# Kernel tuning notes

Hardware: AMD Instinct MI355X
Metric: run time of the kernel (lower is better)

## Reference

```python
import jax, jax.numpy as jnp
import numpy as np

N = 100_000      # nodes
E = 1_600_000    # edges (before self-loops)
IN = 128         # in_dim
H = 4            # heads (layer 1)
C = 32           # hidden_dim (per-head channels)
ED = 16          # edge_dim
NEG_SLOPE = 0.2  # PyG GATConv default


def setup_inputs() -> dict:
    key = jax.random.key(0)
    ks = jax.random.split(key, 16)
    s = 0.05
    return {
        "x": jax.random.normal(ks[0], (N, IN), jnp.float32),
        "edge_index": jax.random.randint(ks[1], (2, E), 0, N, dtype=jnp.int32),
        "edge_attr": jax.random.normal(ks[2], (E, ED), jnp.float32),
        # layer 1 params (heads=H, concat=True)
        "W1": jax.random.normal(ks[3], (IN, H * C), jnp.float32) * s,
        "W1e": jax.random.normal(ks[4], (ED, H * C), jnp.float32) * s,
        "a1_src": jax.random.normal(ks[5], (H, C), jnp.float32) * s,
        "a1_dst": jax.random.normal(ks[6], (H, C), jnp.float32) * s,
        "a1_edge": jax.random.normal(ks[7], (H, C), jnp.float32) * s,
        "b1": jax.random.normal(ks[8], (H * C,), jnp.float32) * s,
        # layer 2 params (heads=1, concat=False)
        "W2": jax.random.normal(ks[9], (H * C, C), jnp.float32) * s,
        "W2e": jax.random.normal(ks[10], (ED, C), jnp.float32) * s,
        "a2_src": jax.random.normal(ks[11], (1, C), jnp.float32) * s,
        "a2_dst": jax.random.normal(ks[12], (1, C), jnp.float32) * s,
        "a2_edge": jax.random.normal(ks[13], (1, C), jnp.float32) * s,
        "b2": jax.random.normal(ks[14], (C,), jnp.float32) * s,
    }


def _add_self_loops(src, dst, edge_attr, n):
    # PyG GATConv: add_self_loops=True, fill_value='mean' -> self-loop edge_attr
    # is the mean of incoming edge attrs per target node.
    deg = jax.ops.segment_sum(jnp.ones_like(dst, jnp.float32), dst, num_segments=n)
    mean_attr = jax.ops.segment_sum(edge_attr, dst, num_segments=n) / jnp.maximum(deg, 1.0)[:, None]
    loop = jnp.arange(n, dtype=src.dtype)
    src2 = jnp.concatenate([src, loop])
    dst2 = jnp.concatenate([dst, loop])
    attr2 = jnp.concatenate([edge_attr, mean_attr], axis=0)
    return src2, dst2, attr2


def _gat_conv(x, src, dst, eattr, W, We, a_s, a_d, a_e, b, concat):
    n = x.shape[0]
    Hh, Cc = a_s.shape
    h = (x @ W).reshape(n, Hh, Cc)                # [N,H,C]
    he = (eattr @ We).reshape(-1, Hh, Cc)          # [E',H,C]
    al_s = jnp.sum(h * a_s, axis=-1)               # [N,H]
    al_d = jnp.sum(h * a_d, axis=-1)               # [N,H]
    al_e = jnp.sum(he * a_e, axis=-1)              # [E',H]
    e = jax.nn.leaky_relu(al_s[src] + al_d[dst] + al_e, NEG_SLOPE)  # [E',H]
    # segment softmax over destination node neighborhoods
    m = jax.ops.segment_max(e, dst, num_segments=n)                 # [N,H]
    p = jnp.exp(e - m[dst])
    z = jax.ops.segment_sum(p, dst, num_segments=n)                 # [N,H]
    alpha = p / z[dst]                                              # [E',H]
    out = jax.ops.segment_sum(alpha[:, :, None] * h[src], dst, num_segments=n)  # [N,H,C]
    if concat:
        out = out.reshape(n, Hh * Cc)
    else:
        out = out.mean(axis=1)
    return out + b, alpha


def reference(x, edge_index, edge_attr,
              W1, W1e, a1_src, a1_dst, a1_edge, b1,
              W2, W2e, a2_src, a2_dst, a2_edge, b2):
    n = x.shape[0]
    src, dst, eattr = _add_self_loops(edge_index[0], edge_index[1], edge_attr, n)
    h1, _ = _gat_conv(x, src, dst, eattr, W1, W1e, a1_src, a1_dst, a1_edge, b1, concat=True)
    h1 = jax.nn.elu(h1)
    # dropout p applied in training only; inference reference -> identity
    h2, alpha2 = _gat_conv(h1, src, dst, eattr, W2, W2e, a2_src, a2_dst, a2_edge, b2, concat=False)
    h2 = jax.nn.elu(h2)
    edge_index_sl = jnp.stack([src, dst])
    return h2, edge_index_sl, alpha2
```

## Files before the change

kernel.cpp:

```cpp
#include <hip/hip_runtime.h>

#define NN 100000
#define NE 1600000
#define NE2 1700000
#define OUT_EI 3200000
#define OUT_AL 6600000
#define SLOPE 0.2f
#define NB 391
#define EPB 6400
#define NBB 250

typedef unsigned short u16;
typedef unsigned int u32;
typedef __bf16 bf16x8 __attribute__((ext_vector_type(8)));
typedef float f32x4 __attribute__((ext_vector_type(4)));
typedef u32 u32x4 __attribute__((ext_vector_type(4)));

__device__ __forceinline__ float bf2f(u16 u){ return __uint_as_float(((u32)u) << 16); }
__device__ __forceinline__ u16 f2bf(float f){
    u32 x = __float_as_uint(f);
    x += 0x7FFFu + ((x >> 16) & 1u);
    return (u16)(x >> 16);
}
__device__ __forceinline__ float eluf(float v){ return v > 0.f ? v : (__expf(v) - 1.f); }
__device__ __forceinline__ float lreluf(float v){ return fmaxf(v, SLOPE * v); }
__device__ __forceinline__ float sel4f(float a, float b, float c, float d, int s){
    float x = (s & 1) ? b : a;
    float y = (s & 1) ? d : c;
    return (s & 2) ? y : x;
}

__global__ __launch_bounds__(256) void k_bhist(const int* __restrict__ ei, int* __restrict__ bcnt){
    __shared__ int s[NB];
    int t = threadIdx.x;
    for (int i = t; i < NB; i += 256) s[i] = 0;
    __syncthreads();
    int e0 = blockIdx.x * EPB;
    for (int i = t; i < EPB; i += 256)
        atomicAdd(&s[ei[NE + e0 + i] >> 8], 1);
    __syncthreads();
    for (int i = t; i < NB; i += 256) if (s[i]) atomicAdd(&bcnt[i], s[i]);
}

__global__ void k_bscan(const int* __restrict__ bcnt, int* __restrict__ bbase, int* __restrict__ bcur){
    __shared__ int s[512];
    int t = threadIdx.x;
    int v = (t < NB) ? bcnt[t] : 0;
    s[t] = v; __syncthreads();
    #pragma unroll
    for (int d = 1; d < 512; d <<= 1){
        int x = (t >= d) ? s[t - d] : 0;
        __syncthreads();
        s[t] += x;
        __syncthreads();
    }
    if (t < NB){ int ex = s[t] - v; bbase[t] = ex; bcur[t] = ex; }
    if (t == 0) bbase[NB] = NE;
}

__global__ __launch_bounds__(256) void k_bscatter(const int* __restrict__ ei, const u16* __restrict__ ale1,
                                                  const u16* __restrict__ ale2,
                                                  int* __restrict__ bcur, u32* __restrict__ binsP,
                                                  uint2* __restrict__ binsA, u16* __restrict__ binsA2){
    __shared__ int cnt[NB];
    __shared__ int base[NB];
    __shared__ int sdst[EPB];
    int t = threadIdx.x;
    for (int i = t; i < NB; i += 256) cnt[i] = 0;
    __syncthreads();
    int e0 = blockIdx.x * EPB;
    for (int i = t; i < EPB; i += 256){
        int dv = ei[NE + e0 + i];
        sdst[i] = dv;
        atomicAdd(&cnt[dv >> 8], 1);
    }
    __syncthreads();
    for (int i = t; i < NB; i += 256){
        int c = cnt[i];
        base[i] = c ? atomicAdd(&bcur[i], c) : 0;
        cnt[i] = 0;
    }
    __syncthreads();
    const uint2* a1 = (const uint2*)ale1;
    for (int i = t; i < EPB; i += 256){
        int e = e0 + i;
        int dst = sdst[i];
        int b = dst >> 8;
        int r = atomicAdd(&cnt[b], 1);
        int pos = base[b] + r;
        binsP[pos] = ((u32)(dst & 255) << 24) | (u32)ei[e];
        binsA[pos] = a1[e];
        binsA2[pos] = ale2[e];
    }
}

__global__ __launch_bounds__(256) void k_fscatter(const u32* __restrict__ binsP, const uint2* __restrict__ binsA,
                                                  const u16* __restrict__ binsA2, const int* __restrict__ bbase,
                                                  int* __restrict__ offsets,
                                                  int* __restrict__ src32, uint2* __restrict__ ale1p,
                                                  u16* __restrict__ ale2p){
    __shared__ int d[256];
    __shared__ int s[256];
    __shared__ int cur[256];
    int t = threadIdx.x, b = blockIdx.x;
    d[t] = 0;
    __syncthreads();
    int bs = bbase[b], be = bbase[b + 1];
    for (int i = bs + t; i < be; i += 256)
        atomicAdd(&d[binsP[i] >> 24], 1);
    __syncthreads();
    int v = d[t];
    s[t] = v; __syncthreads();
    #pragma unroll
    for (int dd = 1; dd < 256; dd <<= 1){
        int x = (t >= dd) ? s[t - dd] : 0;
        __syncthreads();
        s[t] += x;
        __syncthreads();
    }
    int n = b * 256 + t;
    int off = bs + (s[t] - v) + n;
    if (n < NN) offsets[n] = off;
    cur[t] = off + 1;
    if (b == 0 && t == 0) offsets[NN] = NE + NN;
    __syncthreads();
    for (int i = bs + t; i < be; i += 256){
        u32 p = binsP[i];
        int dl = p >> 24;
        int pos = atomicAdd(&cur[dl], 1);
        src32[pos] = (int)(p & 0xFFFFFFu);
        ale1p[pos] = binsA[i];
        ale2p[pos] = binsA2[i];
    }
}

__global__ void k_q(const float* __restrict__ W1e, const float* __restrict__ a1e,
                    const float* __restrict__ W2e, const float* __restrict__ a2e,
                    float* __restrict__ q1, float* __restrict__ q2){
    int t = threadIdx.x;
    int k = t >> 2, h = t & 3;
    float s = 0.f;
    for (int c = 0; c < 32; c++) s += W1e[k * 128 + h * 32 + c] * a1e[h * 32 + c];
    q1[t] = s;
    if (t < 16){
        float s2 = 0.f;
        for (int c = 0; c < 32; c++) s2 += W2e[t * 32 + c] * a2e[c];
        q2[t] = s2;
    }
}

__global__ __launch_bounds__(256) void k_ale(const float* __restrict__ eattr,
                                             const float* __restrict__ q1, const float* __restrict__ q2,
                                             u16* __restrict__ ale1, u16* __restrict__ ale2){
    __shared__ float sq1[64], sq2[16];
    int t = threadIdx.x;
    if (t < 64) sq1[t] = q1[t];
    if (t < 16) sq2[t] = q2[t];
    __syncthreads();
    int gt = blockIdx.x * 256 + t;
    int e = gt >> 2, part = gt & 3;
    f32x4 av = ((const f32x4*)eattr)[(size_t)e * 4 + part];
    int j0 = part * 4;
    float p0 = 0, p1 = 0, p2 = 0, p3 = 0, p4 = 0;
    #pragma unroll
    for (int k = 0; k < 4; k++){
        float a = av[k]; int j = j0 + k;
        p0 += a * sq1[j * 4 + 0]; p1 += a * sq1[j * 4 + 1];
        p2 += a * sq1[j * 4 + 2]; p3 += a * sq1[j * 4 + 3];
        p4 += a * sq2[j];
    }
    #pragma unroll
    for (int m = 1; m < 4; m <<= 1){
        p0 += __shfl_xor(p0, m); p1 += __shfl_xor(p1, m);
        p2 += __shfl_xor(p2, m); p3 += __shfl_xor(p3, m); p4 += __shfl_xor(p4, m);
    }
    if (part == 0){
        ushort4 w; w.x = f2bf(p0); w.y = f2bf(p1); w.z = f2bf(p2); w.w = f2bf(p3);
        ((ushort4*)ale1)[e] = w;
        ale2[e] = f2bf(p4);
    }
}

__global__ __launch_bounds__(256) void k_gemm1(const float* __restrict__ x, const float* __restrict__ W,
                                               const float* __restrict__ a1s, const float* __restrict__ a1d,
                                               u16* __restrict__ h1,
                                               float* __restrict__ al_s, float* __restrict__ al_d){
    __shared__ __align__(16) u16 sW[128 * 136];
    int t = threadIdx.x;
    for (int i = t; i < 128 * 128; i += 256){
        int k = i >> 7, c = i & 127;
        sW[c * 136 + k] = f2bf(W[i]);
    }
    __syncthreads();
    int lane = t & 63, wave = t >> 6;
    int quad = lane >> 4, m16 = lane & 15;
    int rowA = blockIdx.x * 64 + wave * 16 + m16;
    bf16x8 afr[4];
    if (rowA < NN){
        const f32x4* xr = (const f32x4*)(x + (size_t)rowA * 128);
        #pragma unroll
        for (int kk = 0; kk < 4; kk++){
            f32x4 va = xr[kk * 8 + quad * 2];
            f32x4 vb = xr[kk * 8 + quad * 2 + 1];
            #pragma unroll
            for (int i2 = 0; i2 < 4; i2++){ afr[kk][i2] = (__bf16)va[i2]; afr[kk][4 + i2] = (__bf16)vb[i2]; }
        }
    } else {
        #pragma unroll
        for (int kk = 0; kk < 4; kk++)
            #pragma unroll
            for (int i2 = 0; i2 < 8; i2++) afr[kk][i2] = (__bf16)0.f;
    }
    int rowbase = blockIdx.x * 64 + wave * 16 + quad * 4;
    float vsA[4][4], vdA[4][4];
    #pragma unroll
    for (int r = 0; r < 4; r++)
        #pragma unroll
        for (int h = 0; h < 4; h++){ vsA[r][h] = 0.f; vdA[r][h] = 0.f; }
    #pragma unroll
    for (int nt = 0; nt < 8; nt++){
        f32x4 acc = (f32x4){0.f, 0.f, 0.f, 0.f};
        const u16* wp = &sW[(nt * 16 + m16) * 136 + quad * 8];
        #pragma unroll
        for (int kk = 0; kk < 4; kk++){
            bf16x8 bfr = *(const bf16x8*)(wp + kk * 32);
            acc = __builtin_amdgcn_mfma_f32_16x16x32_bf16(afr[kk], bfr, acc, 0, 0, 0);
        }
        int col = nt * 16 + m16;
        float cs = a1s[col], cd = a1d[col];
        const int h = nt >> 1;
        #pragma unroll
        for (int r = 0; r < 4; r++){
            vsA[r][h] += acc[r] * cs;
            vdA[r][h] += acc[r] * cd;
            int row = rowbase + r;
            if (row < NN) h1[(size_t)row * 128 + col] = f2bf(acc[r]);
        }
    }
    #pragma unroll
    for (int r = 0; r < 4; r++)
        #pragma unroll
        for (int h = 0; h < 4; h++)
            #pragma unroll
            for (int m = 1; m < 16; m <<= 1){
                vsA[r][h] += __shfl_xor(vsA[r][h], m);
                vdA[r][h] += __shfl_xor(vdA[r][h], m);
            }
    int rs = m16 >> 2, hs = m16 & 3;
    float s0 = sel4f(vsA[0][0], vsA[0][1], vsA[0][2], vsA[0][3], hs);
    float s1 = sel4f(vsA[1][0], vsA[1][1], vsA[1][2], vsA[1][3], hs);
    float s2 = sel4f(vsA[2][0], vsA[2][1], vsA[2][2], vsA[2][3], hs);
    float s3 = sel4f(vsA[3][0], vsA[3][1], vsA[3][2], vsA[3][3], hs);
    float d0 = sel4f(vdA[0][0], vdA[0][1], vdA[0][2], vdA[0][3], hs);
    float d1 = sel4f(vdA[1][0], vdA[1][1], vdA[1][2], vdA[1][3], hs);
    float d2 = sel4f(vdA[2][0], vdA[2][1], vdA[2][2], vdA[2][3], hs);
    float d3 = sel4f(vdA[3][0], vdA[3][1], vdA[3][2], vdA[3][3], hs);
    float souts = sel4f(s0, s1, s2, s3, rs);
    float soutd = sel4f(d0, d1, d2, d3, rs);
    int row = rowbase + rs;
    if (row < NN){
        al_s[row * 4 + hs] = souts;
        al_d[row * 4 + hs] = soutd;
    }
}

__global__ __launch_bounds__(256) void k_gemm2(const u16* __restrict__ hin, const float* __restrict__ W,
                                               const float* __restrict__ a2s, const float* __restrict__ a2d,
                                               float* __restrict__ h2a,
                                               float* __restrict__ al_s, float* __restrict__ al_d){
    __shared__ __align__(16) u16 sW[32 * 136];
    int t = threadIdx.x;
    for (int i = t; i < 128 * 32; i += 256){
        int k = i >> 5, c = i & 31;
        sW[c * 136 + k] = f2bf(W[i]);
    }
    __syncthreads();
    int lane = t & 63, wave = t >> 6;
    int quad = lane >> 4, m16 = lane & 15;
    int rowA = blockIdx.x * 64 + wave * 16 + m16;
    bf16x8 afr[4];
    if (rowA < NN){
        const u16* xr = hin + (size_t)rowA * 128 + quad * 8;
        #pragma unroll
        for (int kk = 0; kk < 4; kk++) afr[kk] = *(const bf16x8*)(xr + kk * 32);
    } else {
        #pragma unroll
        for (int kk = 0; kk < 4; kk++)
            #pragma unroll
            for (int i2 = 0; i2 < 8; i2++) afr[kk][i2] = (__bf16)0.f;
    }
    int rowbase = blockIdx.x * 64 + wave * 16 + quad * 4;
    float vs2[4], vd2[4];
    #pragma unroll
    for (int r = 0; r < 4; r++){ vs2[r] = 0.f; vd2[r] = 0.f; }
    #pragma unroll
    for (int nt = 0; nt < 2; nt++){
        f32x4 acc = (f32x4){0.f, 0.f, 0.f, 0.f};
        const u16* wp = &sW[(nt * 16 + m16) * 136 + quad * 8];
        #pragma unroll
        for (int kk = 0; kk < 4; kk++){
            bf16x8 bfr = *(const bf16x8*)(wp + kk * 32);
            acc = __builtin_amdgcn_mfma_f32_16x16x32_bf16(afr[kk], bfr, acc, 0, 0, 0);
        }
        int col = nt * 16 + m16;
        float cs = a2s[col], cd = a2d[col];
        #pragma unroll
        for (int r = 0; r < 4; r++){
            vs2[r] += acc[r] * cs;
            vd2[r] += acc[r] * cd;
            int row = rowbase + r;
            if (row < NN) h2a[(size_t)row * 32 + col] = acc[r];
        }
    }
    #pragma unroll
    for (int r = 0; r < 4; r++)
        #pragma unroll
        for (int m = 1; m < 16; m <<= 1){
            vs2[r] += __shfl_xor(vs2[r], m);
            vd2[r] += __shfl_xor(vd2[r], m);
        }
    if (m16 < 4){
        int row = rowbase + m16;
        if (row < NN){
            al_s[row] = sel4f(vs2[0], vs2[1], vs2[2], vs2[3], m16);
            al_d[row] = sel4f(vd2[0], vd2[1], vd2[2], vd2[3], m16);
        }
    }
}

__global__ __launch_bounds__(256) void k_node1(const int* __restrict__ src32, const u16* __restrict__ ale1u,
                                               const int* __restrict__ offsets,
                                               const float* __restrict__ al_s, const float* __restrict__ al_d,
                                               const u16* __restrict__ h1, const float* __restrict__ b1,
                                               u16* __restrict__ h1b){
    int wave = threadIdx.x >> 6, lane = threadIdx.x & 63;
    int n = blockIdx.x * 4 + wave;
    int start = offsets[n], end = offsets[n + 1];
    int degr = end - start - 1;
    int g = lane >> 4, l = lane & 15, hq = l >> 2;
    float aldh = al_d[n * 4 + hq];
    const u32x4* h1v = (const u32x4*)h1;
    float acc[8];
    #pragma unroll
    for (int k = 0; k < 8; k++) acc[k] = 0.f;
    float z = 0.f, sa = 0.f;
    int i = start + 1 + g;
    int src = (i < end) ? __builtin_nontemporal_load(src32 + i) : 0;
    for (; i < end; i += 4){
        int ni = i + 4;
        int nsrc = (ni < end) ? __builtin_nontemporal_load(src32 + ni) : 0;
        float a = bf2f(__builtin_nontemporal_load(ale1u + (size_t)i * 4 + hq));
        float als = al_s[src * 4 + hq];
        u32x4 v = h1v[(size_t)src * 16 + l];
        float e = __expf(lreluf(als + aldh + a));
        z += e; sa += a;
        #pragma unroll
        for (int k = 0; k < 4; k++){
            acc[2 * k]     += e * bf2f((u16)(v[k] & 0xFFFFu));
            acc[2 * k + 1] += e * bf2f((u16)(v[k] >> 16));
        }
        src = nsrc;
    }
    z += __shfl_xor(z, 16); z += __shfl_xor(z, 32);
    sa += __shfl_xor(sa, 16); sa += __shfl_xor(sa, 32);
    float inv_deg = 1.f / fmaxf((float)degr, 1.f);
    float ps = __expf(lreluf(al_s[n * 4 + hq] + aldh + sa * inv_deg));
    z += ps;
    if (g == 0){
        u32x4 v = h1v[(size_t)n * 16 + l];
        #pragma unroll
        for (int k = 0; k < 4; k++){
            acc[2 * k]     += ps * bf2f((u16)(v[k] & 0xFFFFu));
            acc[2 * k + 1] += ps * bf2f((u16)(v[k] >> 16));
        }
    }
    #pragma unroll
    for (int k = 0; k < 8; k++){
        acc[k] += __shfl_xor(acc[k], 16);
        acc[k] += __shfl_xor(acc[k], 32);
    }
    if (g == 0){
        float rz = 1.f / z;
        u32x4 w;
        #pragma unroll
        for (int k = 0; k < 4; k++){
            float v0 = eluf(acc[2 * k]     * rz + b1[l * 8 + 2 * k]);
            float v1 = eluf(acc[2 * k + 1] * rz + b1[l * 8 + 2 * k + 1]);
            w[k] = (u32)f2bf(v0) | ((u32)f2bf(v1) << 16);
        }
        ((u32x4*)h1b)[(size_t)n * 16 + l] = w;
    }
}

__global__ __launch_bounds__(256) void k_node2(const int* __restrict__ src32, const u16* __restrict__ ale2p,
                                               const int* __restrict__ offsets,
                                               const float* __restrict__ al_s, const float* __restrict__ al_d,
                                               const float* __restrict__ h2a, const float* __restrict__ b2,
                                               float* __restrict__ dout, float* __restrict__ rzv){
    int wave = threadIdx.x >> 6, lane = threadIdx.x & 63;
    int n = blockIdx.x * 4 + wave;
    int start = offsets[n], end = offsets[n + 1];
    int degr = end - start - 1;
    float aldn = al_d[n];
    int g = lane >> 3, l = lane & 7;
    const f32x4* h2v = (const f32x4*)h2a;
    f32x4 acc = (f32x4){0.f, 0.f, 0.f, 0.f};
    float z = 0.f, sa = 0.f;
    int i = start + 1 + g;
    int src = (i < end) ? __builtin_nontemporal_load(src32 + i) : 0;
    for (; i < end; i += 8){
        int ni = i + 8;
        int nsrc = (ni < end) ? __builtin_nontemporal_load(src32 + ni) : 0;
        float a = bf2f(__builtin_nontemporal_load(ale2p + i));
        float als = al_s[src];
        f32x4 v = h2v[(size_t)src * 8 + l];
        float e = __expf(lreluf(als + aldn + a));
        z += e; sa += a;
        #pragma unroll
        for (int k = 0; k < 4; k++) acc[k] += e * v[k];
        src = nsrc;
    }
    z += __shfl_xor(z, 8); z += __shfl_xor(z, 16); z += __shfl_xor(z, 32);
    sa += __shfl_xor(sa, 8); sa += __shfl_xor(sa, 16); sa += __shfl_xor(sa, 32);
    float mal = sa / fmaxf((float)degr, 1.f);
    float ps = __expf(lreluf(al_s[n] + aldn + mal));
    z += ps;
    float rz = 1.f / z;
    if (g == 0){
        f32x4 v = h2v[(size_t)n * 8 + l];
        #pragma unroll
        for (int k = 0; k < 4; k++) acc[k] += ps * v[k];
    }
    if (lane == 0){
        rzv[n] = rz;
        dout[OUT_AL + NE + n] = ps * rz;
        dout[OUT_EI + NE + n] = (float)n;
        dout[OUT_EI + NE2 + NE + n] = (float)n;
    }
    #pragma unroll
    for (int k = 0; k < 4; k++){
        acc[k] += __shfl_xor(acc[k], 8);
        acc[k] += __shfl_xor(acc[k], 16);
        acc[k] += __shfl_xor(acc[k], 32);
    }
    if (g == 0){
        f32x4 w;
        #pragma unroll
        for (int k = 0; k < 4; k++) w[k] = eluf(acc[k] + b2[l * 4 + k]);
        ((f32x4*)dout)[(size_t)n * 8 + l] = w;
    }
}

__global__ __launch_bounds__(256) void k_alpha(const int* __restrict__ ei, const u16* __restrict__ ale2,
                                               const float* __restrict__ al_s, const float* __restrict__ al_d,
                                               const float* __restrict__ rzv, float* __restrict__ dout){
    int e = blockIdx.x * 256 + threadIdx.x;
    int src = ei[e], dst = ei[NE + e];
    float a = bf2f(ale2[e]);
    float ev = __expf(lreluf(al_s[src] + al_d[dst] + a));
    __builtin_nontemporal_store(ev * rzv[dst], &dout[OUT_AL + e]);
    __builtin_nontemporal_store((float)src, &dout[OUT_EI + e]);
    __builtin_nontemporal_store((float)dst, &dout[OUT_EI + NE2 + e]);
}

extern "C" void kernel_launch(void* const* d_in, const int* in_sizes, int n_in,
                              void* d_out, int out_size, void* d_ws, size_t ws_size,
                              hipStream_t stream) {
    const float* x     = (const float*)d_in[0];
    const int*   ei    = (const int*)d_in[1];
    const float* eattr = (const float*)d_in[2];
    const float* W1    = (const float*)d_in[3];
    const float* W1e   = (const float*)d_in[4];
    const float* a1s   = (const float*)d_in[5];
    const float* a1d   = (const float*)d_in[6];
    const float* a1e   = (const float*)d_in[7];
    const float* b1    = (const float*)d_in[8];
    const float* W2    = (const float*)d_in[9];
    const float* W2e   = (const float*)d_in[10];
    const float* a2s   = (const float*)d_in[11];
    const float* a2d   = (const float*)d_in[12];
    const float* a2e   = (const float*)d_in[13];
    const float* b2    = (const float*)d_in[14];
    float* dout = (float*)d_out;

    char* ws = (char*)d_ws;
    size_t off = 0;
    auto alloc = [&](size_t bytes) -> void* {
        void* p = ws + off;
        off += (bytes + 255) & ~(size_t)255;
        return p;
    };
    int* bcnt = (int*)alloc((size_t)NB * 4);
    size_t zero_bytes = off;
    int*     offsets = (int*)alloc((size_t)(NN + 1) * 4);
    int*     bbase   = (int*)alloc((size_t)(NB + 1) * 4);
    int*     bcur    = (int*)alloc((size_t)NB * 4);
    u32*     binsP   = (u32*)alloc((size_t)NE * 4);
    uint2*   binsA   = (uint2*)alloc((size_t)NE * 8);
    u16*     binsA2  = (u16*)alloc((size_t)NE * 2);
    int*     src32   = (int*)alloc((size_t)NE2 * 4);
    uint2*   ale1p   = (uint2*)alloc((size_t)NE2 * 8);
    u16*     ale2p   = (u16*)alloc((size_t)NE2 * 2);
    float*   q1      = (float*)alloc(64 * 4);
    float*   q2      = (float*)alloc(16 * 4);
    u16*     ale1    = (u16*)alloc((size_t)NE * 4 * 2);
    u16*     ale2    = (u16*)alloc((size_t)NE * 2);
    float*   al_s1   = (float*)alloc((size_t)NN * 4 * 4);
    float*   al_d1   = (float*)alloc((size_t)NN * 4 * 4);
    u16*     h1      = (u16*)alloc((size_t)NN * 128 * 2);
    u16*     h1b     = (u16*)alloc((size_t)NN * 128 * 2);
    char*  h1r   = (char*)h1;
    float* h2a   = (float*)(h1r);
    float* al_s2 = (float*)(h1r + 12800000);
    float* al_d2 = (float*)(h1r + 13200128);
    float* rzv   = (float*)(h1r + 13600256);

    const int TB = 256;
    hipMemsetAsync(d_ws, 0, zero_bytes, stream);

    k_q<<<1, 64, 0, stream>>>(W1e, a1e, W2e, a2e, q1, q2);
    k_ale<<<NE * 4 / TB, TB, 0, stream>>>(eattr, q1, q2, ale1, ale2);
    k_bhist<<<NBB, TB, 0, stream>>>(ei, bcnt);
    k_bscan<<<1, 512, 0, stream>>>(bcnt, bbase, bcur);
    k_bscatter<<<NBB, TB, 0, stream>>>(ei, ale1, ale2, bcur, binsP, binsA, binsA2);
    k_fscatter<<<NB, TB, 0, stream>>>(binsP, binsA, binsA2, bbase, offsets, src32, ale1p, ale2p);
    k_gemm1<<<(NN + 63) / 64, TB, 0, stream>>>(x, W1, a1s, a1d, h1, al_s1, al_d1);
    k_node1<<<NN / 4, TB, 0, stream>>>(src32, (const u16*)ale1p, offsets, al_s1, al_d1, h1, b1, h1b);
    k_gemm2<<<(NN + 63) / 64, TB, 0, stream>>>(h1b, W2, a2s, a2d, h2a, al_s2, al_d2);
    k_node2<<<NN / 4, TB, 0, stream>>>(src32, ale2p, offsets, al_s2, al_d2, h2a, b2, dout, rzv);
    k_alpha<<<NE / TB, TB, 0, stream>>>(ei, ale2, al_s2, al_d2, rzv, dout);
}
```

Measured before the change: 562.1 us.

## Fuse layer-2 projection into layer-1 aggregation and software-pipeline gather loops

Removes the separate k_gemm2 launch by computing h1 @ W2 and the layer-2 attention logits inside k_node1, using shared-memory copies of W2 and the per-node h1 row. This avoids writing the bf16 h1b buffer and reading it back. The gather loops in both node kernels are restructured to prefetch one edge ahead (source index, logit and feature row), and layer 1 now uses 8 edge groups with 16 channels per lane. The trade-offs are that every block reloads W2 (16 KB) into shared memory, the projection runs as scalar FP32 FMAs instead of MFMA, and a __syncthreads is added. Layer-2 buffers are also re-aliased onto the bin scratch arrays.

Measured after the change: 591.2 us. +5.2%, slower.

```diff
diff --git a/kernel.cpp b/kernel.cpp
--- a/kernel.cpp
+++ b/kernel.cpp
@@ -9,6 +9,7 @@
 #define NB 391
 #define EPB 6400
 #define NBB 250
+#define NNP 100096
 
 typedef unsigned short u16;
 typedef unsigned int u32;
@@ -264,131 +265,106 @@
     }
 }
 
-__global__ __launch_bounds__(256) void k_gemm2(const u16* __restrict__ hin, const float* __restrict__ W,
-                                               const float* __restrict__ a2s, const float* __restrict__ a2d,
-                                               float* __restrict__ h2a,
-                                               float* __restrict__ al_s, float* __restrict__ al_d){
-    __shared__ __align__(16) u16 sW[32 * 136];
-    int t = threadIdx.x;
-    for (int i = t; i < 128 * 32; i += 256){
-        int k = i >> 5, c = i & 31;
-        sW[c * 136 + k] = f2bf(W[i]);
-    }
-    __syncthreads();
-    int lane = t & 63, wave = t >> 6;
-    int quad = lane >> 4, m16 = lane & 15;
-    int rowA = blockIdx.x * 64 + wave * 16 + m16;
-    bf16x8 afr[4];
-    if (rowA < NN){
-        const u16* xr = hin + (size_t)rowA * 128 + quad * 8;
-        #pragma unroll
-        for (int kk = 0; kk < 4; kk++) afr[kk] = *(const bf16x8*)(xr + kk * 32);
-    } else {
-        #pragma unroll
-        for (int kk = 0; kk < 4; kk++)
-            #pragma unroll
-            for (int i2 = 0; i2 < 8; i2++) afr[kk][i2] = (__bf16)0.f;
-    }
-    int rowbase = blockIdx.x * 64 + wave * 16 + quad * 4;
-    float vs2[4], vd2[4];
-    #pragma unroll
-    for (int r = 0; r < 4; r++){ vs2[r] = 0.f; vd2[r] = 0.f; }
-    #pragma unroll
-    for (int nt = 0; nt < 2; nt++){
-        f32x4 acc = (f32x4){0.f, 0.f, 0.f, 0.f};
-        const u16* wp = &sW[(nt * 16 + m16) * 136 + quad * 8];
-        #pragma unroll
-        for (int kk = 0; kk < 4; kk++){
-            bf16x8 bfr = *(const bf16x8*)(wp + kk * 32);
-            acc = __builtin_amdgcn_mfma_f32_16x16x32_bf16(afr[kk], bfr, acc, 0, 0, 0);
-        }
-        int col = nt * 16 + m16;
-        float cs = a2s[col], cd = a2d[col];
-        #pragma unroll
-        for (int r = 0; r < 4; r++){
-            vs2[r] += acc[r] * cs;
-            vd2[r] += acc[r] * cd;
-            int row = rowbase + r;
-            if (row < NN) h2a[(size_t)row * 32 + col] = acc[r];
-        }
-    }
-    #pragma unroll
-    for (int r = 0; r < 4; r++)
-        #pragma unroll
-        for (int m = 1; m < 16; m <<= 1){
-            vs2[r] += __shfl_xor(vs2[r], m);
-            vd2[r] += __shfl_xor(vd2[r], m);
-        }
-    if (m16 < 4){
-        int row = rowbase + m16;
-        if (row < NN){
-            al_s[row] = sel4f(vs2[0], vs2[1], vs2[2], vs2[3], m16);
-            al_d[row] = sel4f(vd2[0], vd2[1], vd2[2], vd2[3], m16);
-        }
-    }
-}
-
 __global__ __launch_bounds__(256) void k_node1(const int* __restrict__ src32, const u16* __restrict__ ale1u,
                                                const int* __restrict__ offsets,
                                                const float* __restrict__ al_s, const float* __restrict__ al_d,
                                                const u16* __restrict__ h1, const float* __restrict__ b1,
-                                               u16* __restrict__ h1b){
-    int wave = threadIdx.x >> 6, lane = threadIdx.x & 63;
+                                               const float* __restrict__ W2,
+                                               const float* __restrict__ a2s, const float* __restrict__ a2d,
+                                               float* __restrict__ h2a,
+                                               float* __restrict__ al_s2, float* __restrict__ al_d2){
+    __shared__ float sW2[128 * 32];
+    __shared__ float sh1[4][128];
+    int t = threadIdx.x;
+    for (int i = t; i < 128 * 32; i += 256) sW2[i] = W2[i];
+    int wave = t >> 6, lane = t & 63;
     int n = blockIdx.x * 4 + wave;
     int start = offsets[n], end = offsets[n + 1];
     int degr = end - start - 1;
-    int g = lane >> 4, l = lane & 15, hq = l >> 2;
+    int g = lane >> 3, l = lane & 7, hq = l >> 1;
     float aldh = al_d[n * 4 + hq];
     const u32x4* h1v = (const u32x4*)h1;
-    float acc[8];
-    #pragma unroll
-    for (int k = 0; k < 8; k++) acc[k] = 0.f;
+    float acc[16];
+    #pragma unroll
+    for (int k = 0; k < 16; k++) acc[k] = 0.f;
     float z = 0.f, sa = 0.f;
     int i = start + 1 + g;
-    int src = (i < end) ? __builtin_nontemporal_load(src32 + i) : 0;
-    for (; i < end; i += 4){
-        int ni = i + 4;
-        int nsrc = (ni < end) ? __builtin_nontemporal_load(src32 + ni) : 0;
-        float a = bf2f(__builtin_nontemporal_load(ale1u + (size_t)i * 4 + hq));
-        float als = al_s[src * 4 + hq];
-        u32x4 v = h1v[(size_t)src * 16 + l];
-        float e = __expf(lreluf(als + aldh + a));
-        z += e; sa += a;
+    int i1 = i + 8, i2 = i + 16;
+    int src0 = (i  < end) ? __builtin_nontemporal_load(src32 + i)  : n;
+    int src1 = (i1 < end) ? __builtin_nontemporal_load(src32 + i1) : n;
+    float a0   = (i < end) ? bf2f(__builtin_nontemporal_load(ale1u + (size_t)i * 4 + hq)) : 0.f;
+    float als0 = al_s[src0 * 4 + hq];
+    u32x4 v00 = h1v[(size_t)src0 * 16 + 2 * l];
+    u32x4 v01 = h1v[(size_t)src0 * 16 + 2 * l + 1];
+    while (i < end){
+        int src2 = (i2 < end) ? __builtin_nontemporal_load(src32 + i2) : n;
+        float a1v   = (i1 < end) ? bf2f(__builtin_nontemporal_load(ale1u + (size_t)i1 * 4 + hq)) : 0.f;
+        float als1 = al_s[src1 * 4 + hq];
+        u32x4 v10 = h1v[(size_t)src1 * 16 + 2 * l];
+        u32x4 v11 = h1v[(size_t)src1 * 16 + 2 * l + 1];
+        float e = __expf(lreluf(als0 + aldh + a0));
+        z += e; sa += a0;
         #pragma unroll
         for (int k = 0; k < 4; k++){
-            acc[2 * k]     += e * bf2f((u16)(v[k] & 0xFFFFu));
-            acc[2 * k + 1] += e * bf2f((u16)(v[k] >> 16));
+            acc[2 * k]     += e * bf2f((u16)(v00[k] & 0xFFFFu));
+            acc[2 * k + 1] += e * bf2f((u16)(v00[k] >> 16));
+            acc[8 + 2 * k] += e * bf2f((u16)(v01[k] & 0xFFFFu));
+            acc[9 + 2 * k] += e * bf2f((u16)(v01[k] >> 16));
         }
-        src = nsrc;
-    }
-    z += __shfl_xor(z, 16); z += __shfl_xor(z, 32);
-    sa += __shfl_xor(sa, 16); sa += __shfl_xor(sa, 32);
+        i = i1; i1 = i2; i2 += 8;
+        src1 = src2; a0 = a1v; als0 = als1; v00 = v10; v01 = v11;
+    }
+    z += __shfl_xor(z, 8); z += __shfl_xor(z, 16); z += __shfl_xor(z, 32);
+    sa += __shfl_xor(sa, 8); sa += __shfl_xor(sa, 16); sa += __shfl_xor(sa, 32);
     float inv_deg = 1.f / fmaxf((float)degr, 1.f);
     float ps = __expf(lreluf(al_s[n * 4 + hq] + aldh + sa * inv_deg));
     z += ps;
     if (g == 0){
-        u32x4 v = h1v[(size_t)n * 16 + l];
+        u32x4 s0 = h1v[(size_t)n * 16 + 2 * l];
+        u32x4 s1 = h1v[(size_t)n * 16 + 2 * l + 1];
         #pragma unroll
         for (int k = 0; k < 4; k++){
-            acc[2 * k]     += ps * bf2f((u16)(v[k] & 0xFFFFu));
-            acc[2 * k + 1] += ps * bf2f((u16)(v[k] >> 16));
+            acc[2 * k]     += ps * bf2f((u16)(s0[k] & 0xFFFFu));
+            acc[2 * k + 1] += ps * bf2f((u16)(s0[k] >> 16));
+            acc[8 + 2 * k] += ps * bf2f((u16)(s1[k] & 0xFFFFu));
+            acc[9 + 2 * k] += ps * bf2f((u16)(s1[k] >> 16));
         }
     }
     #pragma unroll
-    for (int k = 0; k < 8; k++){
+    for (int k = 0; k < 16; k++){
+        acc[k] += __shfl_xor(acc[k], 8);
         acc[k] += __shfl_xor(acc[k], 16);
         acc[k] += __shfl_xor(acc[k], 32);
     }
     if (g == 0){
         float rz = 1.f / z;
-        u32x4 w;
-        #pragma unroll
-        for (int k = 0; k < 4; k++){
-            float v0 = eluf(acc[2 * k]     * rz + b1[l * 8 + 2 * k]);
-            float v1 = eluf(acc[2 * k + 1] * rz + b1[l * 8 + 2 * k + 1]);
-            w[k] = (u32)f2bf(v0) | ((u32)f2bf(v1) << 16);
+        float* dst = &sh1[wave][16 * l];
+        #pragma unroll
+        for (int q = 0; q < 4; q++){
+            f32x4 w;
+            #pragma unroll
+            for (int k = 0; k < 4; k++)
+                w[k] = eluf(acc[4 * q + k] * rz + b1[16 * l + 4 * q + k]);
+            ((f32x4*)dst)[q] = w;
         }
-        ((u32x4*)h1b)[(size_t)n * 16 + l] = w;
+    }
+    __syncthreads();
+    int c = lane & 31, half = lane >> 5;
+    const float* hr = sh1[wave];
+    float s = 0.f;
+    #pragma unroll
+    for (int k = half * 64; k < half * 64 + 64; k += 4){
+        f32x4 hv = *(const f32x4*)(hr + k);
+        s += hv[0] * sW2[(k + 0) * 32 + c] + hv[1] * sW2[(k + 1) * 32 + c]
+           + hv[2] * sW2[(k + 2) * 32 + c] + hv[3] * sW2[(k + 3) * 32 + c];
+    }
+    s += __shfl_xor(s, 32);
+    float vs = s * a2s[c], vd = s * a2d[c];
+    #pragma unroll
+    for (int m = 1; m < 32; m <<= 1){ vs += __shfl_xor(vs, m); vd += __shfl_xor(vd, m); }
+    if (half == 0){
+        h2a[(size_t)n * 32 + c] = s;
+        if (c == 0){ al_s2[n] = vs; al_d2[n] = vd; }
     }
 }
 
@@ -407,18 +383,23 @@
     f32x4 acc = (f32x4){0.f, 0.f, 0.f, 0.f};
     float z = 0.f, sa = 0.f;
     int i = start + 1 + g;
-    int src = (i < end) ? __builtin_nontemporal_load(src32 + i) : 0;
-    for (; i < end; i += 8){
-        int ni = i + 8;
-        int nsrc = (ni < end) ? __builtin_nontemporal_load(src32 + ni) : 0;
-        float a = bf2f(__builtin_nontemporal_load(ale2p + i));
-        float als = al_s[src];
-        f32x4 v = h2v[(size_t)src * 8 + l];
-        float e = __expf(lreluf(als + aldn + a));
-        z += e; sa += a;
-        #pragma unroll
-        for (int k = 0; k < 4; k++) acc[k] += e * v[k];
-        src = nsrc;
+    int i1 = i + 8, i2 = i + 16;
+    int src0 = (i  < end) ? __builtin_nontemporal_load(src32 + i)  : n;
+    int src1 = (i1 < end) ? __builtin_nontemporal_load(src32 + i1) : n;
+    float a0   = (i < end) ? bf2f(__builtin_nontemporal_load(ale2p + i)) : 0.f;
+    float als0 = al_s[src0];
+    f32x4 v0 = h2v[(size_t)src0 * 8 + l];
+    while (i < end){
+        int src2 = (i2 < end) ? __builtin_nontemporal_load(src32 + i2) : n;
+        float a1v   = (i1 < end) ? bf2f(__builtin_nontemporal_load(ale2p + i1)) : 0.f;
+        float als1 = al_s[src1];
+        f32x4 v1 = h2v[(size_t)src1 * 8 + l];
+        float e = __expf(lreluf(als0 + aldn + a0));
+        z += e; sa += a0;
+        #pragma unroll
+        for (int k = 0; k < 4; k++) acc[k] += e * v0[k];
+        i = i1; i1 = i2; i2 += 8;
+        src1 = src2; a0 = a1v; als0 = als1; v0 = v1;
     }
     z += __shfl_xor(z, 8); z += __shfl_xor(z, 16); z += __shfl_xor(z, 32);
     sa += __shfl_xor(sa, 8); sa += __shfl_xor(sa, 16); sa += __shfl_xor(sa, 32);
@@ -508,12 +489,10 @@
     float*   al_s1   = (float*)alloc((size_t)NN * 4 * 4);
     float*   al_d1   = (float*)alloc((size_t)NN * 4 * 4);
     u16*     h1      = (u16*)alloc((size_t)NN * 128 * 2);
-    u16*     h1b     = (u16*)alloc((size_t)NN * 128 * 2);
-    char*  h1r   = (char*)h1;
-    float* h2a   = (float*)(h1r);
-    float* al_s2 = (float*)(h1r + 12800000);
-    float* al_d2 = (float*)(h1r + 13200128);
-    float* rzv   = (float*)(h1r + 13600256);
+    float* h2a   = (float*)binsA;
+    float* al_s2 = (float*)binsP;
+    float* al_d2 = al_s2 + NNP;
+    float* rzv   = al_d2 + NNP;
 
     const int TB = 256;
     hipMemsetAsync(d_ws, 0, zero_bytes, stream);
@@ -525,8 +504,8 @@
     k_bscatter<<<NBB, TB, 0, stream>>>(ei, ale1, ale2, bcur, binsP, binsA, binsA2);
     k_fscatter<<<NB, TB, 0, stream>>>(binsP, binsA, binsA2, bbase, offsets, src32, ale1p, ale2p);
     k_gemm1<<<(NN + 63) / 64, TB, 0, stream>>>(x, W1, a1s, a1d, h1, al_s1, al_d1);
-    k_node1<<<NN / 4, TB, 0, stream>>>(src32, (const u16*)ale1p, offsets, al_s1, al_d1, h1, b1, h1b);
-    k_gemm2<<<(NN + 63) / 64, TB, 0, stream>>>(h1b, W2, a2s, a2d, h2a, al_s2, al_d2);
+    k_node1<<<NN / 4, TB, 0, stream>>>(src32, (const u16*)ale1p, offsets, al_s1, al_d1, h1, b1,
+                                       W2, a2s, a2d, h2a, al_s2, al_d2);
     k_node2<<<NN / 4, TB, 0, stream>>>(src32, ale2p, offsets, al_s2, al_d2, h2a, b2, dout, rzv);
     k_alpha<<<NE / TB, TB, 0, stream>>>(ei, ale2, al_s2, al_d2, rzv, dout);
 }
```
